# Kernel tuning notes

Measured on AMD Instinct MI355X. Metric: run time of the kernel, lower is better.

## Reference

```python
import jax, jax.numpy as jnp
import numpy as np

B, N, DIM, HEADS = 2, 2048, 1024, 16
HD = DIM // HEADS  # 64


def _rope_table(n, hd):
    pos = jnp.arange(n, dtype=jnp.float32)
    inv_freq = 1.0 / (10000.0 ** (jnp.arange(0, hd, 2, dtype=jnp.float32) / hd))
    ang = pos[:, None] * inv_freq[None, :]                 # [n, hd/2]
    return jnp.stack([jnp.cos(ang), jnp.sin(ang)], -1)      # [n, hd/2, 2]


def setup_inputs() -> dict:
    key = jax.random.key(0)
    ks = jax.random.split(key, 5)
    s = 0.02
    return {
        "x": jax.random.normal(ks[0], (B, N, DIM), jnp.float32),
        "rope": _rope_table(N, HD),
        "qkv_w": jax.random.normal(ks[1], (3 * DIM, DIM), jnp.float32) * s,
        "qkv_b": jax.random.normal(ks[2], (3 * DIM,), jnp.float32) * s,
        "proj_w": jax.random.normal(ks[3], (DIM, DIM), jnp.float32) * s,
        "proj_b": jax.random.normal(ks[4], (DIM,), jnp.float32) * s,
    }


def _apply_rotary(t, rope):
    # t: [b, h, n, d]; rope: [n, d/2, 2] holding (cos, sin)
    b, h, n, d = t.shape
    t2 = t.reshape(b, h, n, d // 2, 2)
    x1, x2 = t2[..., 0], t2[..., 1]
    cos, sin = rope[..., 0], rope[..., 1]                    # [n, d/2]
    o1 = x1 * cos - x2 * sin
    o2 = x1 * sin + x2 * cos
    return jnp.stack([o1, o2], -1).reshape(b, h, n, d)


def reference(x, rope, qkv_w, qkv_b, proj_w, proj_b):
    b, n, ch = x.shape
    qkv = x @ qkv_w.T + qkv_b                                # [b, n, 3*dim]
    qkv = qkv.reshape(b, n, 3, HEADS, HD)
    qkv = jnp.transpose(qkv, (2, 0, 3, 1, 4))                # [3, b, h, n, d]
    q, k, v = qkv[0], qkv[1], qkv[2]
    q = _apply_rotary(q, rope)
    k = _apply_rotary(k, rope)
    scale = 1.0 / jnp.sqrt(jnp.float32(HD))
    scores = jnp.einsum('bhqd,bhkd->bhqk', q, k) * scale     # [b, h, n, n]
    attn = jax.nn.softmax(scores, axis=-1)
    o = jnp.einsum('bhqk,bhkd->bhqd', attn, v)               # [b, h, n, d]
    o = jnp.transpose(o, (0, 2, 1, 3)).reshape(b, n, ch)
    return o @ proj_w.T + proj_b
```

## Files before the change

### kernel.cpp

```cpp
#include <hip/hip_runtime.h>
#include <math.h>

#define NB   2
#define SEQ  2048
#define NDIM 1024
#define NH   16
#define HD   64

using bf16x8 = __attribute__((ext_vector_type(8))) short;
using f32x4  = __attribute__((ext_vector_type(4))) float;

__device__ __forceinline__ unsigned short f2bf(float f) {
    union { float f; unsigned int u; } v; v.f = f;
    unsigned int r = v.u + 0x7fffu + ((v.u >> 16) & 1u);
    return (unsigned short)(r >> 16);
}

__global__ __launch_bounds__(256) void cast_bf16_kernel(
    const float* __restrict__ in, unsigned short* __restrict__ out, int n4)
{
    int i = blockIdx.x * 256 + threadIdx.x;
    if (i < n4) {
        float4 f = ((const float4*)in)[i];
        ushort4 u;
        u.x = f2bf(f.x); u.y = f2bf(f.y); u.z = f2bf(f.z); u.w = f2bf(f.w);
        ((ushort4*)out)[i] = u;
    }
}

__global__ __launch_bounds__(256) void qkv_gemm_kernel(
    const unsigned short* __restrict__ A,
    const unsigned short* __restrict__ W,
    const float* __restrict__ bias,
    const float* __restrict__ rope,
    unsigned short* __restrict__ Qw, unsigned short* __restrict__ Kw,
    unsigned short* __restrict__ Vw)
{
    __shared__ __align__(16) unsigned short As[128][40];
    __shared__ __align__(16) unsigned short Ws[128][40];
    const int tid  = threadIdx.x;
    const int lane = tid & 63;
    const int wv   = tid >> 6;
    const int wr   = wv >> 1, wc = wv & 1;
    const int l15  = lane & 15, lg = lane >> 4;
    const int mbase = blockIdx.y * 128, nbase = blockIdx.x * 128;
    const int srow = tid >> 1, shalf = tid & 1;

    f32x4 acc[4][4] = {};

    const unsigned short* ap = &A[(size_t)(mbase + srow) * 1024 + shalf * 16];
    const unsigned short* wp = &W[(size_t)(nbase + srow) * 1024 + shalf * 16];

    for (int k0 = 0; k0 < 1024; k0 += 32) {
        bf16x8 a0 = *(const bf16x8*)(ap + k0);
        bf16x8 a1 = *(const bf16x8*)(ap + k0 + 8);
        bf16x8 w0 = *(const bf16x8*)(wp + k0);
        bf16x8 w1 = *(const bf16x8*)(wp + k0 + 8);
        *(bf16x8*)&As[srow][shalf * 16]     = a0;
        *(bf16x8*)&As[srow][shalf * 16 + 8] = a1;
        *(bf16x8*)&Ws[srow][shalf * 16]     = w0;
        *(bf16x8*)&Ws[srow][shalf * 16 + 8] = w1;
        __syncthreads();
        bf16x8 af[4], bfr[4];
#pragma unroll
        for (int mf = 0; mf < 4; ++mf)
            af[mf] = *(const bf16x8*)&As[wr * 64 + mf * 16 + l15][lg * 8];
#pragma unroll
        for (int nf = 0; nf < 4; ++nf)
            bfr[nf] = *(const bf16x8*)&Ws[wc * 64 + nf * 16 + l15][lg * 8];
#pragma unroll
        for (int mf = 0; mf < 4; ++mf)
#pragma unroll
            for (int nf = 0; nf < 4; ++nf)
                acc[mf][nf] = __builtin_amdgcn_mfma_f32_16x16x32_bf16(
                    af[mf], bfr[nf], acc[mf][nf], 0, 0, 0);
        __syncthreads();
    }

#pragma unroll
    for (int mf = 0; mf < 4; ++mf) {
#pragma unroll
        for (int r = 0; r < 4; ++r) {
            int m   = mbase + wr * 64 + mf * 16 + lg * 4 + r;
            int bb  = m >> 11;
            int tok = m & 2047;
#pragma unroll
            for (int nf = 0; nf < 4; ++nf) {
                int c = nbase + wc * 64 + nf * 16 + l15;
                float val = acc[mf][nf][r] + bias[c];
                float partner = __shfl_xor(val, 1, 64);
                int sel = c >> 10;
                int hh  = (c >> 6) & 15;
                int d   = c & 63;
                float res = val;
                if (sel < 2) {
                    float cs = rope[((size_t)tok * 32 + (d >> 1)) * 2 + 0];
                    float sn = rope[((size_t)tok * 32 + (d >> 1)) * 2 + 1];
                    if (d & 1) res = partner * sn + val * cs;
                    else       res = val * cs - partner * sn;
                }
                if (sel == 0) res *= 0.18033688011112042f;
                unsigned short* dst = (sel == 0) ? Qw : (sel == 1) ? Kw : Vw;
                dst[((size_t)(bb * NH + hh) * SEQ + tok) * HD + d] = f2bf(res);
            }
        }
    }
}

__global__ __launch_bounds__(256) void attn_mfma_kernel(
    const unsigned short* __restrict__ Qw, const unsigned short* __restrict__ Kw,
    const unsigned short* __restrict__ Vw, unsigned short* __restrict__ AO)
{
    __shared__ __align__(16) unsigned short Vt[64][64];
    __shared__ __align__(16) unsigned short Ps[4][16][64];

    const int tid  = threadIdx.x;
    const int lane = tid & 63;
    const int wq   = tid >> 6;
    const int l15  = lane & 15, lg = lane >> 4;
    const int qbase = blockIdx.x * 64;
    const int hh = blockIdx.y, bb = blockIdx.z;

    const unsigned short* Qb = Qw + (size_t)(bb * NH + hh) * SEQ * HD;
    const unsigned short* Kb = Kw + (size_t)(bb * NH + hh) * SEQ * HD;
    const unsigned short* Vb = Vw + (size_t)(bb * NH + hh) * SEQ * HD;

    bf16x8 qf[2];
#pragma unroll
    for (int ks = 0; ks < 2; ++ks)
        qf[ks] = *(const bf16x8*)&Qb[(size_t)(qbase + wq * 16 + l15) * HD + ks * 32 + lg * 8];

    f32x4 o[4] = {};
    float lrow = 0.f;

    const int kp = tid & 31;
    const int dc = tid >> 5;

    for (int kt = 0; kt < SEQ; kt += 64) {
        __syncthreads();
        {
            bf16x8 va  = *(const bf16x8*)&Vb[(size_t)(kt + 2 * kp) * HD + dc * 8];
            bf16x8 vb_ = *(const bf16x8*)&Vb[(size_t)(kt + 2 * kp + 1) * HD + dc * 8];
#pragma unroll
            for (int e = 0; e < 8; ++e) {
                int d = dc * 8 + e;
                unsigned int pk = (unsigned int)(unsigned short)va[e]
                                | ((unsigned int)(unsigned short)vb_[e] << 16);
                int ob = (kp * 4) ^ ((d & 7) << 4);
                *(unsigned int*)((char*)&Vt[d][0] + ob) = pk;
            }
        }
        __syncthreads();

        f32x4 st[4] = {};
#pragma unroll
        for (int kf = 0; kf < 4; ++kf)
#pragma unroll
            for (int ks = 0; ks < 2; ++ks) {
                bf16x8 kfr = *(const bf16x8*)&Kb[(size_t)(kt + kf * 16 + l15) * HD + ks * 32 + lg * 8];
                st[kf] = __builtin_amdgcn_mfma_f32_16x16x32_bf16(kfr, qf[ks], st[kf], 0, 0, 0);
            }

        float p[16];
        float rs = 0.f;
#pragma unroll
        for (int kf = 0; kf < 4; ++kf)
#pragma unroll
            for (int r = 0; r < 4; ++r) {
                float e_ = __builtin_amdgcn_exp2f(st[kf][r]);
                p[kf * 4 + r] = e_;
                rs += e_;
            }
        rs += __shfl_xor(rs, 16, 64);
        rs += __shfl_xor(rs, 32, 64);
        lrow += rs;

#pragma unroll
        for (int kf = 0; kf < 4; ++kf) {
            ushort4 w;
            w.x = f2bf(p[kf * 4 + 0]); w.y = f2bf(p[kf * 4 + 1]);
            w.z = f2bf(p[kf * 4 + 2]); w.w = f2bf(p[kf * 4 + 3]);
            int ob = (kf * 32 + lg * 8) ^ ((l15 & 7) << 4);
            *(ushort4*)((char*)&Ps[wq][l15][0] + ob) = w;
        }

#pragma unroll
        for (int df = 0; df < 4; ++df) {
            const int d = df * 16 + l15;
#pragma unroll
            for (int ks = 0; ks < 2; ++ks) {
                int op = (ks * 64 + lg * 16) ^ ((l15 & 7) << 4);
                bf16x8 pf = *(const bf16x8*)((const char*)&Ps[wq][l15][0] + op);
                bf16x8 vf = *(const bf16x8*)((const char*)&Vt[d][0] + op);
                o[df] = __builtin_amdgcn_mfma_f32_16x16x32_bf16(pf, vf, o[df], 0, 0, 0);
            }
        }
    }

#pragma unroll
    for (int r = 0; r < 4; ++r) {
        float linv = 1.0f / __shfl(lrow, lg * 4 + r, 64);
        int q = qbase + wq * 16 + lg * 4 + r;
#pragma unroll
        for (int df = 0; df < 4; ++df)
            AO[(size_t)(bb * SEQ + q) * NDIM + hh * HD + df * 16 + l15] =
                f2bf(o[df][r] * linv);
    }
}

__global__ __launch_bounds__(256) void proj_gemm_kernel(
    const unsigned short* __restrict__ A,
    const unsigned short* __restrict__ W,
    const float* __restrict__ bias,
    float* __restrict__ out)
{
    __shared__ __align__(16) unsigned short As[128][40];
    __shared__ __align__(16) unsigned short Ws[128][40];
    const int tid  = threadIdx.x;
    const int lane = tid & 63;
    const int wv   = tid >> 6;
    const int wr   = wv >> 1, wc = wv & 1;
    const int l15  = lane & 15, lg = lane >> 4;
    const int mbase = blockIdx.y * 128, nbase = blockIdx.x * 128;
    const int srow = tid >> 1, shalf = tid & 1;

    f32x4 acc[4][4] = {};

    const unsigned short* ap = &A[(size_t)(mbase + srow) * 1024 + shalf * 16];
    const unsigned short* wp = &W[(size_t)(nbase + srow) * 1024 + shalf * 16];

    for (int k0 = 0; k0 < 1024; k0 += 32) {
        bf16x8 a0 = *(const bf16x8*)(ap + k0);
        bf16x8 a1 = *(const bf16x8*)(ap + k0 + 8);
        bf16x8 w0 = *(const bf16x8*)(wp + k0);
        bf16x8 w1 = *(const bf16x8*)(wp + k0 + 8);
        *(bf16x8*)&As[srow][shalf * 16]     = a0;
        *(bf16x8*)&As[srow][shalf * 16 + 8] = a1;
        *(bf16x8*)&Ws[srow][shalf * 16]     = w0;
        *(bf16x8*)&Ws[srow][shalf * 16 + 8] = w1;
        __syncthreads();
        bf16x8 af[4], bfr[4];
#pragma unroll
        for (int mf = 0; mf < 4; ++mf)
            af[mf] = *(const bf16x8*)&As[wr * 64 + mf * 16 + l15][lg * 8];
#pragma unroll
        for (int nf = 0; nf < 4; ++nf)
            bfr[nf] = *(const bf16x8*)&Ws[wc * 64 + nf * 16 + l15][lg * 8];
#pragma unroll
        for (int mf = 0; mf < 4; ++mf)
#pragma unroll
            for (int nf = 0; nf < 4; ++nf)
                acc[mf][nf] = __builtin_amdgcn_mfma_f32_16x16x32_bf16(
                    af[mf], bfr[nf], acc[mf][nf], 0, 0, 0);
        __syncthreads();
    }

#pragma unroll
    for (int mf = 0; mf < 4; ++mf) {
#pragma unroll
        for (int r = 0; r < 4; ++r) {
            int m = mbase + wr * 64 + mf * 16 + lg * 4 + r;
#pragma unroll
            for (int nf = 0; nf < 4; ++nf) {
                int c = nbase + wc * 64 + nf * 16 + l15;
                out[(size_t)m * 1024 + c] = acc[mf][nf][r] + bias[c];
            }
        }
    }
}

extern "C" void kernel_launch(void* const* d_in, const int* in_sizes, int n_in,
                              void* d_out, int out_size, void* d_ws, size_t ws_size,
                              hipStream_t stream)
{
    (void)in_sizes; (void)n_in; (void)out_size; (void)ws_size;
    const float* x      = (const float*)d_in[0];
    const float* rope   = (const float*)d_in[1];
    const float* qkv_w  = (const float*)d_in[2];
    const float* qkv_b  = (const float*)d_in[3];
    const float* proj_w = (const float*)d_in[4];
    const float* proj_b = (const float*)d_in[5];
    float* out = (float*)d_out;

    unsigned short* ws = (unsigned short*)d_ws;
    const size_t M1 = 1024 * 1024;
    unsigned short* xb     = ws;
    unsigned short* qkvwb  = ws + 4 * M1;
    unsigned short* projwb = ws + 7 * M1;
    unsigned short* Qw     = ws + 8 * M1;
    unsigned short* Kw     = ws + 12 * M1;
    unsigned short* Vw     = ws + 16 * M1;
    unsigned short* AO     = ws + 20 * M1;

    cast_bf16_kernel<<<4096, 256, 0, stream>>>(x, xb, 1048576);
    cast_bf16_kernel<<<3072, 256, 0, stream>>>(qkv_w, qkvwb, 786432);
    cast_bf16_kernel<<<1024, 256, 0, stream>>>(proj_w, projwb, 262144);

    qkv_gemm_kernel<<<dim3(24, 32), 256, 0, stream>>>(
        xb, qkvwb, qkv_b, rope, Qw, Kw, Vw);
    attn_mfma_kernel<<<dim3(SEQ / 64, NH, NB), 256, 0, stream>>>(Qw, Kw, Vw, AO);
    proj_gemm_kernel<<<dim3(8, 32), 256, 0, stream>>>(AO, projwb, proj_b, out);
}
```

Before: 310.4 us.

## Software-pipeline K/V loads with double-buffered V tile in attention

The attention loop now prefetches the next K tile into registers and the V tile two steps ahead. The transposed V tile is double-buffered in shared memory, so each iteration needs one barrier instead of two and global load latency overlaps with the MFMA and exp work. Launch bounds request 3 blocks per SM, and the loop is unrolled by two to ping-pong the register buffers. The cost is higher register pressure from 16 K fragments plus V registers held live, which could cause spills under the occupancy hint.

```diff
diff --git a/kernel.cpp b/kernel.cpp
--- a/kernel.cpp
+++ b/kernel.cpp
@@ -107,11 +107,11 @@
     }
 }
 
-__global__ __launch_bounds__(256) void attn_mfma_kernel(
+__global__ __launch_bounds__(256, 3) void attn_mfma_kernel(
     const unsigned short* __restrict__ Qw, const unsigned short* __restrict__ Kw,
     const unsigned short* __restrict__ Vw, unsigned short* __restrict__ AO)
 {
-    __shared__ __align__(16) unsigned short Vt[64][64];
+    __shared__ __align__(16) unsigned short Vt[2][64][64];
     __shared__ __align__(16) unsigned short Ps[4][16][64];
 
     const int tid  = threadIdx.x;
@@ -136,40 +136,56 @@
     const int kp = tid & 31;
     const int dc = tid >> 5;
 
-    for (int kt = 0; kt < SEQ; kt += 64) {
-        __syncthreads();
-        {
-            bf16x8 va  = *(const bf16x8*)&Vb[(size_t)(kt + 2 * kp) * HD + dc * 8];
-            bf16x8 vb_ = *(const bf16x8*)&Vb[(size_t)(kt + 2 * kp + 1) * HD + dc * 8];
-#pragma unroll
-            for (int e = 0; e < 8; ++e) {
-                int d = dc * 8 + e;
-                unsigned int pk = (unsigned int)(unsigned short)va[e]
-                                | ((unsigned int)(unsigned short)vb_[e] << 16);
-                int ob = (kp * 4) ^ ((d & 7) << 4);
-                *(unsigned int*)((char*)&Vt[d][0] + ob) = pk;
-            }
-        }
-        __syncthreads();
-
+    bf16x8 ka[8], kb2[8];
+    bf16x8 vr0, vr1;
+
+    auto loadK = [&](bf16x8 (&kr)[8], int kt) {
+#pragma unroll
+        for (int kf = 0; kf < 4; ++kf)
+#pragma unroll
+            for (int ks = 0; ks < 2; ++ks)
+                kr[kf * 2 + ks] = *(const bf16x8*)
+                    &Kb[(size_t)(kt + kf * 16 + l15) * HD + ks * 32 + lg * 8];
+    };
+    auto loadV = [&](int kt) {
+        vr0 = *(const bf16x8*)&Vb[(size_t)(kt + 2 * kp) * HD + dc * 8];
+        vr1 = *(const bf16x8*)&Vb[(size_t)(kt + 2 * kp + 1) * HD + dc * 8];
+    };
+    auto writeV = [&](int buf) {
+#pragma unroll
+        for (int e = 0; e < 8; ++e) {
+            int d = dc * 8 + e;
+            unsigned int pk = (unsigned int)(unsigned short)vr0[e]
+                            | ((unsigned int)(unsigned short)vr1[e] << 16);
+            int ob = (kp * 4) ^ ((d & 7) << 4);
+            *(unsigned int*)((char*)&Vt[buf][d][0] + ob) = pk;
+        }
+    };
+
+    loadV(0);
+    loadK(ka, 0);
+    writeV(0);
+    loadV(64);
+    __syncthreads();
+
+    auto tile = [&](int t, bf16x8 (&kcur)[8], bf16x8 (&knxt)[8], int cur) {
         f32x4 st[4] = {};
 #pragma unroll
         for (int kf = 0; kf < 4; ++kf)
 #pragma unroll
-            for (int ks = 0; ks < 2; ++ks) {
-                bf16x8 kfr = *(const bf16x8*)&Kb[(size_t)(kt + kf * 16 + l15) * HD + ks * 32 + lg * 8];
-                st[kf] = __builtin_amdgcn_mfma_f32_16x16x32_bf16(kfr, qf[ks], st[kf], 0, 0, 0);
-            }
-
-        float p[16];
+            for (int ks = 0; ks < 2; ++ks)
+                st[kf] = __builtin_amdgcn_mfma_f32_16x16x32_bf16(
+                    kcur[kf * 2 + ks], qf[ks], st[kf], 0, 0, 0);
+
+        if (t + 1 < SEQ / 64) loadK(knxt, (t + 1) * 64);
+
         float rs = 0.f;
 #pragma unroll
         for (int kf = 0; kf < 4; ++kf)
 #pragma unroll
             for (int r = 0; r < 4; ++r) {
-                float e_ = __builtin_amdgcn_exp2f(st[kf][r]);
-                p[kf * 4 + r] = e_;
-                rs += e_;
+                st[kf][r] = __builtin_amdgcn_exp2f(st[kf][r]);
+                rs += st[kf][r];
             }
         rs += __shfl_xor(rs, 16, 64);
         rs += __shfl_xor(rs, 32, 64);
@@ -178,8 +194,8 @@
 #pragma unroll
         for (int kf = 0; kf < 4; ++kf) {
             ushort4 w;
-            w.x = f2bf(p[kf * 4 + 0]); w.y = f2bf(p[kf * 4 + 1]);
-            w.z = f2bf(p[kf * 4 + 2]); w.w = f2bf(p[kf * 4 + 3]);
+            w.x = f2bf(st[kf][0]); w.y = f2bf(st[kf][1]);
+            w.z = f2bf(st[kf][2]); w.w = f2bf(st[kf][3]);
             int ob = (kf * 32 + lg * 8) ^ ((l15 & 7) << 4);
             *(ushort4*)((char*)&Ps[wq][l15][0] + ob) = w;
         }
@@ -191,10 +207,19 @@
             for (int ks = 0; ks < 2; ++ks) {
                 int op = (ks * 64 + lg * 16) ^ ((l15 & 7) << 4);
                 bf16x8 pf = *(const bf16x8*)((const char*)&Ps[wq][l15][0] + op);
-                bf16x8 vf = *(const bf16x8*)((const char*)&Vt[d][0] + op);
+                bf16x8 vf = *(const bf16x8*)((const char*)&Vt[cur][d][0] + op);
                 o[df] = __builtin_amdgcn_mfma_f32_16x16x32_bf16(pf, vf, o[df], 0, 0, 0);
             }
         }
+
+        if (t + 1 < SEQ / 64) writeV(cur ^ 1);
+        if (t + 2 < SEQ / 64) loadV((t + 2) * 64);
+        __syncthreads();
+    };
+
+    for (int i = 0; i < SEQ / 128; ++i) {
+        tile(2 * i,     ka,  kb2, 0);
+        tile(2 * i + 1, kb2, ka,  1);
     }
 
 #pragma unroll
```

Result: no change. 311.0 us (+0.2%).
